# Kernel tuning notes

Hardware: AMD Instinct MI355X
Metric: run time of the kernel (lower is better)

Reference implementation:

```python
import jax, jax.numpy as jnp
import numpy as np

B, S, D, H = 8, 1024, 1024, 16
HD = D // H  # head_dim = 64
SCALE = HD ** -0.5


def setup_inputs() -> dict:
    key = jax.random.key(0)
    ks = jax.random.split(key, 10)
    std = D ** -0.5
    return {
        "hidden_states": jax.random.normal(ks[0], (B, S, D), jnp.float32),
        "attn_mask": jnp.zeros((B, 1, S, S), jnp.float32),
        "prev_attn_weights": jax.random.normal(ks[1], (B, H, S, S), jnp.float32),
        "Wq": jax.random.normal(ks[2], (D, D), jnp.float32) * std,
        "bq": jnp.zeros((D,), jnp.float32),
        "Wk": jax.random.normal(ks[3], (D, D), jnp.float32) * std,
        "bk": jnp.zeros((D,), jnp.float32),
        "Wv": jax.random.normal(ks[4], (D, D), jnp.float32) * std,
        "bv": jnp.zeros((D,), jnp.float32),
    }


def _split_heads(x):
    # (B, S, D) -> (B, H, S, HD)
    return x.reshape(B, S, H, HD).transpose(0, 2, 1, 3)


def reference(hidden_states, attn_mask, prev_attn_weights, Wq, bq, Wk, bk, Wv, bv):
    q = _split_heads(hidden_states @ Wq + bq)
    k = _split_heads(hidden_states @ Wk + bk)
    v = _split_heads(hidden_states @ Wv + bv)
    # scaled dot-product scores + additive mask + realformer residual scores
    scores = jnp.einsum("bhqd,bhkd->bhqk", q, k) * SCALE
    scores = scores + attn_mask + prev_attn_weights
    probs = jax.nn.softmax(scores, axis=-1)  # dropout p=0 (eval)
    ctx = jnp.einsum("bhqk,bhkd->bhqd", probs, v)
    # (B, H, S, HD) -> (B, S, D)
    out = ctx.transpose(0, 2, 1, 3).reshape(B, S, D)
    return out
```

## Files before the change

### kernel.cpp

```cpp
#include <hip/hip_runtime.h>

#define B_  8
#define S_  1024
#define D_  1024
#define H_  16
#define HD_ 64
#define M_  8192
#define LOG2E 1.44269504088896f
#define QSCALE_ (0.125f * 1.44269504088896f)
#define MSHIFT_ 20.0f

typedef __attribute__((ext_vector_type(8))) short bf16x8;
typedef __attribute__((ext_vector_type(4))) float f32x4;

__device__ __forceinline__ unsigned short f2b(float x) {
  union { float f; unsigned u; } un; un.f = x;
  unsigned r = un.u + 0x7FFFu + ((un.u >> 16) & 1u);
  return (unsigned short)(r >> 16);
}

__global__ __launch_bounds__(256) void k_convert_x(const float* __restrict__ x,
                                                   unsigned short* __restrict__ o) {
  int i = (blockIdx.x * 256 + threadIdx.x) * 4;
  const int n = M_ * D_;
  const int stride = gridDim.x * 256 * 4;
  for (; i < n; i += stride) {
    const float4 v = *(const float4*)(x + i);
    ushort4 r;
    r.x = f2b(v.x); r.y = f2b(v.y); r.z = f2b(v.z); r.w = f2b(v.w);
    *(ushort4*)(o + i) = r;
  }
}

__global__ __launch_bounds__(256) void k_transpose_w(const float* __restrict__ Wq,
    const float* __restrict__ Wk, const float* __restrict__ Wv,
    unsigned short* __restrict__ Wt) {
  __shared__ float t[64][65];
  const float* W = (blockIdx.z == 0) ? Wq : ((blockIdx.z == 1) ? Wk : Wv);
  unsigned short* dst = Wt + (size_t)blockIdx.z * (D_ * D_);
  const int k0 = blockIdx.x * 64, n0 = blockIdx.y * 64;
  const int tid = threadIdx.x;
#pragma unroll
  for (int i = 0; i < 16; ++i) {
    const int lin = i * 256 + tid;
    const int r = lin >> 6, c = lin & 63;
    t[r][c] = W[(size_t)(k0 + r) * D_ + n0 + c];
  }
  __syncthreads();
#pragma unroll
  for (int i = 0; i < 16; ++i) {
    const int lin = i * 256 + tid;
    const int r = lin >> 6, c = lin & 63;
    dst[(size_t)(n0 + r) * D_ + k0 + c] = f2b(t[c][r]);
  }
}

template <int MODE>
__global__ __launch_bounds__(256) void k_proj(const unsigned short* __restrict__ X,
    const unsigned short* __restrict__ Wt,
    const float* __restrict__ bq, const float* __restrict__ bk, const float* __restrict__ bv,
    unsigned short* __restrict__ Qw, unsigned short* __restrict__ Kw,
    unsigned short* __restrict__ Vt) {
  __shared__ unsigned short xs[128 * 32];
  __shared__ unsigned short wsh[128 * 32];
  const int tid = threadIdx.x;
  const int lane = tid & 63, wv = tid >> 6;
  const int g = lane >> 4, li = lane & 15;
  const int m0 = blockIdx.x * 128;
  const int n0 = blockIdx.y * 128;
  const int wr = wv >> 1, wc = wv & 1;
  const int wtrow0 = (MODE == 0) ? n0 : (2048 + n0);

  f32x4 acc[4][4];
#pragma unroll
  for (int i = 0; i < 4; ++i)
#pragma unroll
    for (int j = 0; j < 4; ++j) acc[i][j] = (f32x4){0.f, 0.f, 0.f, 0.f};

  const int srow = wv * 32 + (lane >> 2);
  const int skel = (lane & 3) * 8;

  for (int k0 = 0; k0 < D_; k0 += 32) {
#pragma unroll
    for (int i = 0; i < 2; ++i) {
      const unsigned short* gx = X + (size_t)(m0 + srow + i * 16) * D_ + k0 + skel;
      const unsigned short* gw = Wt + (size_t)(wtrow0 + srow + i * 16) * D_ + k0 + skel;
      __builtin_amdgcn_global_load_lds(
          (const __attribute__((address_space(1))) void*)gx,
          (__attribute__((address_space(3))) void*)&xs[(wv * 32 + i * 16) * 32], 16, 0, 0);
      __builtin_amdgcn_global_load_lds(
          (const __attribute__((address_space(1))) void*)gw,
          (__attribute__((address_space(3))) void*)&wsh[(wv * 32 + i * 16) * 32], 16, 0, 0);
    }
    __syncthreads();
    bf16x8 af[4], bfr[4];
#pragma unroll
    for (int i = 0; i < 4; ++i) {
      const int ar = wr * 64 + i * 16 + li;
      const int br = wc * 64 + i * 16 + li;
      if (MODE == 0) {
        af[i]  = *(const bf16x8*)&xs[ar * 32 + g * 8];
        bfr[i] = *(const bf16x8*)&wsh[br * 32 + g * 8];
      } else {
        af[i]  = *(const bf16x8*)&wsh[ar * 32 + g * 8];
        bfr[i] = *(const bf16x8*)&xs[br * 32 + g * 8];
      }
    }
#pragma unroll
    for (int i = 0; i < 4; ++i)
#pragma unroll
      for (int j = 0; j < 4; ++j)
        acc[i][j] = __builtin_amdgcn_mfma_f32_16x16x32_bf16(af[i], bfr[j], acc[i][j], 0, 0, 0);
    __syncthreads();
  }

  if (MODE == 0) {
#pragma unroll
    for (int j = 0; j < 4; ++j) {
      const int n = n0 + wc * 64 + j * 16 + li;
      const float bias = (n < D_) ? bq[n] : bk[n - D_];
#pragma unroll
      for (int i = 0; i < 4; ++i) {
#pragma unroll
        for (int r = 0; r < 4; ++r) {
          const int m = m0 + wr * 64 + i * 16 + g * 4 + r;
          const float v = acc[i][j][r] + bias;
          const int bb = m >> 10, ss = m & 1023;
          if (n < D_) {
            Qw[((size_t)(bb * H_ + (n >> 6)) * S_ + ss) * HD_ + (n & 63)] = f2b(v * QSCALE_);
          } else {
            const int nk = n - D_;
            Kw[((size_t)(bb * H_ + (nk >> 6)) * S_ + ss) * HD_ + (nk & 63)] = f2b(v);
          }
        }
      }
    }
  } else {
#pragma unroll
    for (int i = 0; i < 4; ++i) {
#pragma unroll
      for (int r = 0; r < 4; ++r) {
        const int nv = n0 + wr * 64 + i * 16 + g * 4 + r;
        const float bias = bv[nv];
#pragma unroll
        for (int j = 0; j < 4; ++j) {
          const int m = m0 + wc * 64 + j * 16 + li;
          const int bb = m >> 10, ss = m & 1023;
          const float v = acc[i][j][r] + bias;
          Vt[((size_t)(bb * H_ + (nv >> 6)) * HD_ + (nv & 63)) * S_ + ss] = f2b(v);
        }
      }
    }
  }
}

__global__ __launch_bounds__(256, 2) void k_attn(const unsigned short* __restrict__ Qw,
    const unsigned short* __restrict__ Kw, const unsigned short* __restrict__ Vt,
    const float* __restrict__ prev, const float* __restrict__ mask,
    float* __restrict__ out) {
  __shared__ unsigned short k_s[2][4096];
  __shared__ unsigned short v_s[2][4096];
  __shared__ float pm_s[2][4][4][64][4];
  __shared__ unsigned short p_lds[4][16][72];
  const int tid = threadIdx.x;
  const int lane = tid & 63, wv = tid >> 6;
  const int g = lane >> 4, li = lane & 15;

  const int phys = blockIdx.x + 16 * blockIdx.y;
  const int b  = phys & 7;
  const int qt = (phys >> 3) & 15;
  const int h  = phys >> 7;
  const int bh = b * H_ + h;
  const int q0 = qt * 64 + wv * 16;

  const float* pdma = prev + (size_t)bh * S_ * S_ + (size_t)(q0 + li) * S_ + g * 4;
  const float* mb   = mask + (size_t)b * S_ * S_ + (size_t)(q0 + li) * S_ + g * 4;
  const unsigned short* kbase = Kw + (size_t)bh * S_ * HD_;
  const unsigned short* vbase = Vt + (size_t)bh * HD_ * S_;

  bf16x8 qf[2];
  {
    const unsigned short* qp = Qw + ((size_t)bh * S_ + q0 + li) * HD_ + g * 8;
    qf[0] = *(const bf16x8*)qp;
    qf[1] = *(const bf16x8*)(qp + 32);
  }

  const int dr0 = (0 * 256 + tid) >> 3, dc0 = (0 * 256 + tid) & 7;
  const int dr1 = (1 * 256 + tid) >> 3, dc1 = (1 * 256 + tid) & 7;
  const int sc0 = ((dc0 ^ (dr0 & 7)) << 3);
  const int sc1 = ((dc1 ^ (dr1 & 7)) << 3);

#define STAGE(TN, BI)                                                                      \
  {                                                                                        \
    const int sn = (TN) * 64;                                                              \
    __builtin_amdgcn_global_load_lds(                                                      \
        (const __attribute__((address_space(1))) void*)(kbase + (size_t)(sn + dr0) * HD_ + sc0), \
        (__attribute__((address_space(3))) void*)(&k_s[BI][0] + wv * 512), 16, 0, 0);      \
    __builtin_amdgcn_global_load_lds(                                                      \
        (const __attribute__((address_space(1))) void*)(kbase + (size_t)(sn + dr1) * HD_ + sc1), \
        (__attribute__((address_space(3))) void*)(&k_s[BI][0] + 2048 + wv * 512), 16, 0, 0); \
    __builtin_amdgcn_global_load_lds(                                                      \
        (const __attribute__((address_space(1))) void*)(vbase + (size_t)dr0 * S_ + sn + sc0), \
        (__attribute__((address_space(3))) void*)(&v_s[BI][0] + wv * 512), 16, 0, 0);      \
    __builtin_amdgcn_global_load_lds(                                                      \
        (const __attribute__((address_space(1))) void*)(vbase + (size_t)dr1 * S_ + sn + sc1), \
        (__attribute__((address_space(3))) void*)(&v_s[BI][0] + 2048 + wv * 512), 16, 0, 0); \
    _Pragma("unroll")                                                                      \
    for (int cb = 0; cb < 4; ++cb)                                                         \
      __builtin_amdgcn_global_load_lds(                                                    \
          (const __attribute__((address_space(1))) void*)(pdma + sn + cb * 16),            \
          (__attribute__((address_space(3))) void*)&pm_s[BI][wv][cb][0][0], 16, 0, 2);     \
  }

  float lrun = 0.f;
  f32x4 ctx[4];
#pragma unroll
  for (int d = 0; d < 4; ++d) ctx[d] = (f32x4){0.f, 0.f, 0.f, 0.f};

  f32x4 mA[4], mB[4];

  STAGE(0, 0);
#pragma unroll
  for (int cb = 0; cb < 4; ++cb) mA[cb] = *(const f32x4*)(mb + cb * 16);

#define PHASE(T, PB, NB, MCUR, MNXT)                                                  \
  {                                                                                   \
    const int tn = ((T) < 15) ? (T) + 1 : 15;                                         \
    STAGE(tn, NB);                                                                    \
    _Pragma("unroll")                                                                 \
    for (int cb = 0; cb < 4; ++cb)                                                    \
      MNXT[cb] = *(const f32x4*)(mb + tn * 64 + cb * 16);                             \
    asm volatile("s_waitcnt vmcnt(12)" ::: "memory");                                 \
    __builtin_amdgcn_s_barrier();                                                     \
    {                                                                                 \
      const unsigned short* kb = &k_s[PB][0];                                         \
      const unsigned short* vb = &v_s[PB][0];                                         \
      f32x4 sa[4];                                                                    \
      _Pragma("unroll")                                                               \
      for (int cb = 0; cb < 4; ++cb) {                                                \
        const int r = cb * 16 + li;                                                   \
        const bf16x8 k0 = *(const bf16x8*)(kb + r * 64 + ((g ^ (li & 7)) << 3));      \
        const bf16x8 k1 = *(const bf16x8*)(kb + r * 64 + (((g + 4) ^ (li & 7)) << 3)); \
        f32x4 z = (f32x4){0.f, 0.f, 0.f, 0.f};                                        \
        z      = __builtin_amdgcn_mfma_f32_16x16x32_bf16(k0, qf[0], z, 0, 0, 0);      \
        sa[cb] = __builtin_amdgcn_mfma_f32_16x16x32_bf16(k1, qf[1], z, 0, 0, 0);      \
      }                                                                               \
      _Pragma("unroll")                                                               \
      for (int cb = 0; cb < 4; ++cb) {                                                \
        const f32x4 pv = *(const f32x4*)&pm_s[PB][wv][cb][lane][0];                   \
        f32x4 pmc;                                                                    \
        pmc.x = fmaf(pv.x + MCUR[cb].x, LOG2E, -MSHIFT_);                             \
        pmc.y = fmaf(pv.y + MCUR[cb].y, LOG2E, -MSHIFT_);                             \
        pmc.z = fmaf(pv.z + MCUR[cb].z, LOG2E, -MSHIFT_);                             \
        pmc.w = fmaf(pv.w + MCUR[cb].w, LOG2E, -MSHIFT_);                             \
        const float e0 = exp2f(sa[cb][0] + pmc.x);                                    \
        const float e1 = exp2f(sa[cb][1] + pmc.y);                                    \
        const float e2 = exp2f(sa[cb][2] + pmc.z);                                    \
        const float e3 = exp2f(sa[cb][3] + pmc.w);                                    \
        lrun += (e0 + e1) + (e2 + e3);                                                \
        ushort4 pw;                                                                   \
        pw.x = f2b(e0); pw.y = f2b(e1); pw.z = f2b(e2); pw.w = f2b(e3);               \
        *(ushort4*)&p_lds[wv][li][cb * 16 + g * 4] = pw;                              \
      }                                                                               \
      bf16x8 pf0 = *(const bf16x8*)&p_lds[wv][li][g * 8];                             \
      bf16x8 pf1 = *(const bf16x8*)&p_lds[wv][li][32 + g * 8];                        \
      _Pragma("unroll")                                                               \
      for (int d = 0; d < 4; ++d) {                                                   \
        const int r = d * 16 + li;                                                    \
        const bf16x8 v0 = *(const bf16x8*)(vb + r * 64 + ((g ^ (li & 7)) << 3));      \
        const bf16x8 v1 = *(const bf16x8*)(vb + r * 64 + (((g + 4) ^ (li & 7)) << 3)); \
        ctx[d] = __builtin_amdgcn_mfma_f32_16x16x32_bf16(pf0, v0, ctx[d], 0, 0, 0);   \
        ctx[d] = __builtin_amdgcn_mfma_f32_16x16x32_bf16(pf1, v1, ctx[d], 0, 0, 0);   \
      }                                                                               \
    }                                                                                 \
    __builtin_amdgcn_s_barrier();                                                     \
  }

  for (int t = 0; t < 16; t += 2) {
    PHASE(t,     0, 1, mA, mB);
    PHASE(t + 1, 1, 0, mB, mA);
  }
#undef PHASE
#undef STAGE

  lrun += __shfl_xor(lrun, 16);
  lrun += __shfl_xor(lrun, 32);
#pragma unroll
  for (int j = 0; j < 4; ++j) {
    const float rs = __shfl(lrun, g * 4 + j);
    const float inv = 1.0f / rs;
    const int q = q0 + g * 4 + j;
    float* op = out + ((size_t)b * S_ + q) * D_ + h * HD_ + li;
#pragma unroll
    for (int d = 0; d < 4; ++d)
      op[d * 16] = ctx[d][j] * inv;
  }
}

extern "C" void kernel_launch(void* const* d_in, const int* in_sizes, int n_in,
                              void* d_out, int out_size, void* d_ws, size_t ws_size,
                              hipStream_t stream) {
  const float* hs   = (const float*)d_in[0];
  const float* mask = (const float*)d_in[1];
  const float* prev = (const float*)d_in[2];
  const float* Wq   = (const float*)d_in[3];
  const float* bq   = (const float*)d_in[4];
  const float* Wk   = (const float*)d_in[5];
  const float* bk   = (const float*)d_in[6];
  const float* Wv   = (const float*)d_in[7];
  const float* bv   = (const float*)d_in[8];
  float* out = (float*)d_out;

  char* ws = (char*)d_ws;
  unsigned short* Xbf = (unsigned short*)ws;
  unsigned short* Wt  = (unsigned short*)(ws + (16ull << 20));
  unsigned short* Qw  = (unsigned short*)(ws + (22ull << 20));
  unsigned short* Kw  = (unsigned short*)(ws + (38ull << 20));
  unsigned short* Vt  = (unsigned short*)(ws + (54ull << 20));

  k_convert_x<<<2048, 256, 0, stream>>>(hs, Xbf);
  k_transpose_w<<<dim3(16, 16, 3), 256, 0, stream>>>(Wq, Wk, Wv, Wt);
  k_proj<0><<<dim3(64, 16), 256, 0, stream>>>(Xbf, Wt, bq, bk, bv, Qw, Kw, Vt);
  k_proj<1><<<dim3(64, 8),  256, 0, stream>>>(Xbf, Wt, bq, bk, bv, Qw, Kw, Vt);
  k_attn<<<dim3(16, 128), 256, 0, stream>>>(Qw, Kw, Vt, prev, mask, out);
}
```

Baseline: 291.2 us.

## Split attention key dimension across waves, drop per-tile barriers, reduce via LDS

Work is now split among the four waves by key subset instead of by query rows. Each wave processes all 64 queries of the block against its own 16-key slice of each tile, so there is no cross-wave dependency inside the loop and the two s_barriers per tile are removed. P is fed to the MFMA directly from registers, zero-padded to half-K, with no LDS round-trip. Partial contexts and row sums are combined through LDS at the end. In exchange, half of each PV MFMA multiplies zeros, register pressure rises from 16 context accumulators, and correctness now depends on each wave only reading LDS data it staged itself.

```diff
diff --git a/kernel.cpp b/kernel.cpp
--- a/kernel.cpp
+++ b/kernel.cpp
@@ -11,6 +11,7 @@
 #define MSHIFT_ 20.0f
 
 typedef __attribute__((ext_vector_type(8))) short bf16x8;
+typedef __attribute__((ext_vector_type(4))) short bf16x4;
 typedef __attribute__((ext_vector_type(4))) float f32x4;
 
 __device__ __forceinline__ unsigned short f2b(float x) {
@@ -158,10 +159,7 @@
     const unsigned short* __restrict__ Kw, const unsigned short* __restrict__ Vt,
     const float* __restrict__ prev, const float* __restrict__ mask,
     float* __restrict__ out) {
-  __shared__ unsigned short k_s[2][4096];
-  __shared__ unsigned short v_s[2][4096];
-  __shared__ float pm_s[2][4][4][64][4];
-  __shared__ unsigned short p_lds[4][16][72];
+  __shared__ __align__(16) char smem[66560];
   const int tid = threadIdx.x;
   const int lane = tid & 63, wv = tid >> 6;
   const int g = lane >> 4, li = lane & 15;
@@ -171,109 +169,103 @@
   const int qt = (phys >> 3) & 15;
   const int h  = phys >> 7;
   const int bh = b * H_ + h;
-  const int q0 = qt * 64 + wv * 16;
-
-  const float* pdma = prev + (size_t)bh * S_ * S_ + (size_t)(q0 + li) * S_ + g * 4;
-  const float* mb   = mask + (size_t)b * S_ * S_ + (size_t)(q0 + li) * S_ + g * 4;
+
   const unsigned short* kbase = Kw + (size_t)bh * S_ * HD_;
   const unsigned short* vbase = Vt + (size_t)bh * HD_ * S_;
-
-  bf16x8 qf[2];
-  {
-    const unsigned short* qp = Qw + ((size_t)bh * S_ + q0 + li) * HD_ + g * 8;
-    qf[0] = *(const bf16x8*)qp;
-    qf[1] = *(const bf16x8*)(qp + 32);
-  }
-
-  const int dr0 = (0 * 256 + tid) >> 3, dc0 = (0 * 256 + tid) & 7;
-  const int dr1 = (1 * 256 + tid) >> 3, dc1 = (1 * 256 + tid) & 7;
-  const int sc0 = ((dc0 ^ (dr0 & 7)) << 3);
-  const int sc1 = ((dc1 ^ (dr1 & 7)) << 3);
+  const float* pbase = prev + (size_t)bh * S_ * S_ + (size_t)(qt * 64 + li) * S_ + wv * 16 + g * 4;
+  const float* mb    = mask + (size_t)b * S_ * S_ + (size_t)(qt * 64 + li) * S_ + wv * 16 + g * 4;
+
+  const int koff = (wv * 16 + (lane >> 3)) * HD_ + (((lane & 7) ^ (lane >> 3)) << 3);
+  const int voff = (lane >> 1) * S_ + wv * 16 + ((lane & 1) << 3);
+
+  bf16x8 qA[4], qB[4];
+#pragma unroll
+  for (int qb = 0; qb < 4; ++qb) {
+    const unsigned short* qp = Qw + ((size_t)bh * S_ + qt * 64 + qb * 16 + li) * HD_ + g * 8;
+    qA[qb] = *(const bf16x8*)qp;
+    qB[qb] = *(const bf16x8*)(qp + 32);
+  }
 
 #define STAGE(TN, BI)                                                                      \
   {                                                                                        \
-    const int sn = (TN) * 64;                                                              \
+    const int t64 = (TN) * 64;                                                             \
     __builtin_amdgcn_global_load_lds(                                                      \
-        (const __attribute__((address_space(1))) void*)(kbase + (size_t)(sn + dr0) * HD_ + sc0), \
-        (__attribute__((address_space(3))) void*)(&k_s[BI][0] + wv * 512), 16, 0, 0);      \
+        (const __attribute__((address_space(1))) void*)(kbase + (size_t)t64 * HD_ + koff), \
+        (__attribute__((address_space(3))) void*)(smem + (BI) * 8192 + wv * 2048), 16, 0, 0); \
     __builtin_amdgcn_global_load_lds(                                                      \
-        (const __attribute__((address_space(1))) void*)(kbase + (size_t)(sn + dr1) * HD_ + sc1), \
-        (__attribute__((address_space(3))) void*)(&k_s[BI][0] + 2048 + wv * 512), 16, 0, 0); \
+        (const __attribute__((address_space(1))) void*)(kbase + (size_t)t64 * HD_ + koff + 512), \
+        (__attribute__((address_space(3))) void*)(smem + (BI) * 8192 + wv * 2048 + 1024), 16, 0, 0); \
     __builtin_amdgcn_global_load_lds(                                                      \
-        (const __attribute__((address_space(1))) void*)(vbase + (size_t)dr0 * S_ + sn + sc0), \
-        (__attribute__((address_space(3))) void*)(&v_s[BI][0] + wv * 512), 16, 0, 0);      \
+        (const __attribute__((address_space(1))) void*)(vbase + voff + t64),               \
+        (__attribute__((address_space(3))) void*)(smem + 16384 + (BI) * 8192 + wv * 2048), 16, 0, 0); \
     __builtin_amdgcn_global_load_lds(                                                      \
-        (const __attribute__((address_space(1))) void*)(vbase + (size_t)dr1 * S_ + sn + sc1), \
-        (__attribute__((address_space(3))) void*)(&v_s[BI][0] + 2048 + wv * 512), 16, 0, 0); \
+        (const __attribute__((address_space(1))) void*)(vbase + voff + 32 * S_ + t64),     \
+        (__attribute__((address_space(3))) void*)(smem + 16384 + (BI) * 8192 + wv * 2048 + 1024), 16, 0, 0); \
     _Pragma("unroll")                                                                      \
-    for (int cb = 0; cb < 4; ++cb)                                                         \
+    for (int pq = 0; pq < 4; ++pq)                                                         \
       __builtin_amdgcn_global_load_lds(                                                    \
-          (const __attribute__((address_space(1))) void*)(pdma + sn + cb * 16),            \
-          (__attribute__((address_space(3))) void*)&pm_s[BI][wv][cb][0][0], 16, 0, 2);     \
-  }
-
-  float lrun = 0.f;
-  f32x4 ctx[4];
-#pragma unroll
-  for (int d = 0; d < 4; ++d) ctx[d] = (f32x4){0.f, 0.f, 0.f, 0.f};
+          (const __attribute__((address_space(1))) void*)(pbase + (size_t)pq * 16 * S_ + t64), \
+          (__attribute__((address_space(3))) void*)(smem + 32768 + (BI) * 16384 + wv * 4096 + pq * 1024), 16, 0, 0); \
+  }
+
+  float lrun[4] = {0.f, 0.f, 0.f, 0.f};
+  f32x4 ctx[4][4];
+#pragma unroll
+  for (int d = 0; d < 4; ++d)
+#pragma unroll
+    for (int q = 0; q < 4; ++q) ctx[d][q] = (f32x4){0.f, 0.f, 0.f, 0.f};
 
   f32x4 mA[4], mB[4];
 
   STAGE(0, 0);
 #pragma unroll
-  for (int cb = 0; cb < 4; ++cb) mA[cb] = *(const f32x4*)(mb + cb * 16);
+  for (int qb = 0; qb < 4; ++qb) mA[qb] = *(const f32x4*)(mb + (size_t)qb * 16 * S_);
 
 #define PHASE(T, PB, NB, MCUR, MNXT)                                                  \
   {                                                                                   \
     const int tn = ((T) < 15) ? (T) + 1 : 15;                                         \
     STAGE(tn, NB);                                                                    \
     _Pragma("unroll")                                                                 \
-    for (int cb = 0; cb < 4; ++cb)                                                    \
-      MNXT[cb] = *(const f32x4*)(mb + tn * 64 + cb * 16);                             \
+    for (int qb = 0; qb < 4; ++qb)                                                    \
+      MNXT[qb] = *(const f32x4*)(mb + (size_t)qb * 16 * S_ + tn * 64);                \
     asm volatile("s_waitcnt vmcnt(12)" ::: "memory");                                 \
-    __builtin_amdgcn_s_barrier();                                                     \
+    __builtin_amdgcn_sched_barrier(0);                                                \
     {                                                                                 \
-      const unsigned short* kb = &k_s[PB][0];                                         \
-      const unsigned short* vb = &v_s[PB][0];                                         \
+      const char* kb  = smem + (PB) * 8192 + wv * 2048;                               \
+      const char* vb  = smem + 16384 + (PB) * 8192 + wv * 2048;                       \
+      const char* pmw = smem + 32768 + (PB) * 16384 + wv * 4096;                      \
+      const bf16x8 kf0 = *(const bf16x8*)(kb + li * 128 + ((g ^ (li & 7)) << 4));     \
+      const bf16x8 kf1 = *(const bf16x8*)(kb + li * 128 + (((4 + g) ^ (li & 7)) << 4)); \
       f32x4 sa[4];                                                                    \
       _Pragma("unroll")                                                               \
-      for (int cb = 0; cb < 4; ++cb) {                                                \
-        const int r = cb * 16 + li;                                                   \
-        const bf16x8 k0 = *(const bf16x8*)(kb + r * 64 + ((g ^ (li & 7)) << 3));      \
-        const bf16x8 k1 = *(const bf16x8*)(kb + r * 64 + (((g + 4) ^ (li & 7)) << 3)); \
+      for (int qb = 0; qb < 4; ++qb) {                                                \
         f32x4 z = (f32x4){0.f, 0.f, 0.f, 0.f};                                        \
-        z      = __builtin_amdgcn_mfma_f32_16x16x32_bf16(k0, qf[0], z, 0, 0, 0);      \
-        sa[cb] = __builtin_amdgcn_mfma_f32_16x16x32_bf16(k1, qf[1], z, 0, 0, 0);      \
+        z      = __builtin_amdgcn_mfma_f32_16x16x32_bf16(kf0, qA[qb], z, 0, 0, 0);    \
+        sa[qb] = __builtin_amdgcn_mfma_f32_16x16x32_bf16(kf1, qB[qb], z, 0, 0, 0);    \
+      }                                                                               \
+      bf16x8 pk[4];                                                                   \
+      _Pragma("unroll")                                                               \
+      for (int qb = 0; qb < 4; ++qb) {                                                \
+        const f32x4 pv = *(const f32x4*)(pmw + qb * 1024 + lane * 16);                \
+        const float e0 = exp2f(sa[qb][0] + fmaf(pv[0] + MCUR[qb][0], LOG2E, -MSHIFT_)); \
+        const float e1 = exp2f(sa[qb][1] + fmaf(pv[1] + MCUR[qb][1], LOG2E, -MSHIFT_)); \
+        const float e2 = exp2f(sa[qb][2] + fmaf(pv[2] + MCUR[qb][2], LOG2E, -MSHIFT_)); \
+        const float e3 = exp2f(sa[qb][3] + fmaf(pv[3] + MCUR[qb][3], LOG2E, -MSHIFT_)); \
+        lrun[qb] += (e0 + e1) + (e2 + e3);                                            \
+        union { unsigned short s[8]; bf16x8 v; } c8;                                  \
+        c8.s[0] = f2b(e0); c8.s[1] = f2b(e1); c8.s[2] = f2b(e2); c8.s[3] = f2b(e3);   \
+        c8.s[4] = 0; c8.s[5] = 0; c8.s[6] = 0; c8.s[7] = 0;                           \
+        pk[qb] = c8.v;                                                                \
       }                                                                               \
       _Pragma("unroll")                                                               \
-      for (int cb = 0; cb < 4; ++cb) {                                                \
-        const f32x4 pv = *(const f32x4*)&pm_s[PB][wv][cb][lane][0];                   \
-        f32x4 pmc;                                                                    \
-        pmc.x = fmaf(pv.x + MCUR[cb].x, LOG2E, -MSHIFT_);                             \
-        pmc.y = fmaf(pv.y + MCUR[cb].y, LOG2E, -MSHIFT_);                             \
-        pmc.z = fmaf(pv.z + MCUR[cb].z, LOG2E, -MSHIFT_);                             \
-        pmc.w = fmaf(pv.w + MCUR[cb].w, LOG2E, -MSHIFT_);                             \
-        const float e0 = exp2f(sa[cb][0] + pmc.x);                                    \
-        const float e1 = exp2f(sa[cb][1] + pmc.y);                                    \
-        const float e2 = exp2f(sa[cb][2] + pmc.z);                                    \
-        const float e3 = exp2f(sa[cb][3] + pmc.w);                                    \
-        lrun += (e0 + e1) + (e2 + e3);                                                \
-        ushort4 pw;                                                                   \
-        pw.x = f2b(e0); pw.y = f2b(e1); pw.z = f2b(e2); pw.w = f2b(e3);               \
-        *(ushort4*)&p_lds[wv][li][cb * 16 + g * 4] = pw;                              \
-      }                                                                               \
-      bf16x8 pf0 = *(const bf16x8*)&p_lds[wv][li][g * 8];                             \
-      bf16x8 pf1 = *(const bf16x8*)&p_lds[wv][li][32 + g * 8];                        \
-      _Pragma("unroll")                                                               \
-      for (int d = 0; d < 4; ++d) {                                                   \
-        const int r = d * 16 + li;                                                    \
-        const bf16x8 v0 = *(const bf16x8*)(vb + r * 64 + ((g ^ (li & 7)) << 3));      \
-        const bf16x8 v1 = *(const bf16x8*)(vb + r * 64 + (((g + 4) ^ (li & 7)) << 3)); \
-        ctx[d] = __builtin_amdgcn_mfma_f32_16x16x32_bf16(pf0, v0, ctx[d], 0, 0, 0);   \
-        ctx[d] = __builtin_amdgcn_mfma_f32_16x16x32_bf16(pf1, v1, ctx[d], 0, 0, 0);   \
+      for (int db = 0; db < 4; ++db) {                                                \
+        const bf16x4 v4 = *(const bf16x4*)(vb + (db * 16 + li) * 32 + g * 8);         \
+        const bf16x8 vf = (bf16x8){v4[0], v4[1], v4[2], v4[3], 0, 0, 0, 0};           \
+        _Pragma("unroll")                                                             \
+        for (int qb = 0; qb < 4; ++qb)                                                \
+          ctx[db][qb] = __builtin_amdgcn_mfma_f32_16x16x32_bf16(vf, pk[qb], ctx[db][qb], 0, 0, 0); \
       }                                                                               \
     }                                                                                 \
-    __builtin_amdgcn_s_barrier();                                                     \
   }
 
   for (int t = 0; t < 16; t += 2) {
@@ -283,17 +275,45 @@
 #undef PHASE
 #undef STAGE
 
-  lrun += __shfl_xor(lrun, 16);
-  lrun += __shfl_xor(lrun, 32);
-#pragma unroll
-  for (int j = 0; j < 4; ++j) {
-    const float rs = __shfl(lrun, g * 4 + j);
-    const float inv = 1.0f / rs;
-    const int q = q0 + g * 4 + j;
-    float* op = out + ((size_t)b * S_ + q) * D_ + h * HD_ + li;
-#pragma unroll
-    for (int d = 0; d < 4; ++d)
-      op[d * 16] = ctx[d][j] * inv;
+  asm volatile("s_waitcnt vmcnt(0)" ::: "memory");
+  __builtin_amdgcn_sched_barrier(0);
+  __syncthreads();
+
+  float* ex = (float*)smem;
+#pragma unroll
+  for (int db = 0; db < 4; ++db)
+#pragma unroll
+    for (int qb = 0; qb < 4; ++qb)
+      *(f32x4*)(ex + ((((wv * 4 + db) * 4 + qb) * 64) + lane) * 4) = ctx[db][qb];
+
+#pragma unroll
+  for (int qb = 0; qb < 4; ++qb) {
+    lrun[qb] += __shfl_xor(lrun[qb], 16);
+    lrun[qb] += __shfl_xor(lrun[qb], 32);
+  }
+  float* ls = (float*)(smem + 65536);
+  if (g == 0) {
+#pragma unroll
+    for (int qb = 0; qb < 4; ++qb) ls[(wv * 4 + qb) * 16 + li] = lrun[qb];
+  }
+  __syncthreads();
+
+#pragma unroll
+  for (int qb = 0; qb < 4; ++qb) {
+    const float tot = ls[(0 * 4 + qb) * 16 + li] + ls[(1 * 4 + qb) * 16 + li] +
+                      ls[(2 * 4 + qb) * 16 + li] + ls[(3 * 4 + qb) * 16 + li];
+    const float inv = 1.0f / tot;
+    f32x4 a0 = *(const f32x4*)(ex + ((((0 * 4 + wv) * 4 + qb) * 64) + lane) * 4);
+    f32x4 a1 = *(const f32x4*)(ex + ((((1 * 4 + wv) * 4 + qb) * 64) + lane) * 4);
+    f32x4 a2 = *(const f32x4*)(ex + ((((2 * 4 + wv) * 4 + qb) * 64) + lane) * 4);
+    f32x4 a3 = *(const f32x4*)(ex + ((((3 * 4 + wv) * 4 + qb) * 64) + lane) * 4);
+    float4 o;
+    o.x = (a0[0] + a1[0] + a2[0] + a3[0]) * inv;
+    o.y = (a0[1] + a1[1] + a2[1] + a3[1]) * inv;
+    o.z = (a0[2] + a1[2] + a2[2] + a3[2]) * inv;
+    o.w = (a0[3] + a1[3] + a2[3] + a3[3]) * inv;
+    *(float4*)(out + ((size_t)(b * S_ + qt * 64 + qb * 16 + li)) * D_ +
+               h * HD_ + wv * 16 + g * 4) = o;
   }
 }
 
```

After: 320.4 us. 1.1x slower.
